# Optimization experiments

Measured on AMD Instinct MI355X. Metric: run time of the kernel, lower is better.

Reference implementation:

```python
import jax, jax.numpy as jnp
import numpy as np

D = 64       # feature_dim
C = 64       # number of classes
NS = 1024    # support samples (16 shots per class)
NQ = 32768   # query samples
REG = 0.3    # reg_param
KAPPA0 = 1.0 / 600.0  # gamma_m from _num_images=600


def _l2norm(x):
    # torch F.normalize(p=2, dim=1) with eps=1e-12
    return x / jnp.maximum(jnp.linalg.norm(x, axis=1, keepdims=True), 1e-12)


def setup_inputs() -> dict:
    key = jax.random.key(0)
    k1, k2 = jax.random.split(key)
    return {
        "X_support": jax.random.normal(k1, (NS, D), dtype=jnp.float32),
        "y_support": jnp.arange(NS, dtype=jnp.int32) % C,  # every class populated
        "X_query": jax.random.normal(k2, (NQ, D), dtype=jnp.float32),
        "m": jnp.zeros((D,), dtype=jnp.float32),            # zeros * gamma_m
        "S": jnp.eye(D, dtype=jnp.float32),                  # eye * gamma_S
        "nu": jnp.float32(float(D)),
        "kappa": jnp.float32(KAPPA0),
    }


def reference(X_support, y_support, X_query, m, S, nu, kappa):
    # ---- fit ----
    Xs = _l2norm(X_support)                                   # [NS, D]
    onehot = jax.nn.one_hot(y_support, C, dtype=Xs.dtype)     # [NS, C]
    Nj = onehot.sum(axis=0)                                   # [C] per-class counts
    means = (onehot.T @ Xs) / Nj[:, None]                     # [C, D] class means
    N0 = Nj[0]                                                # original uses class-0 count
    # head_mu_eq is vector + scalar broadcast, exactly as the torch code
    head = kappa / (kappa + N0) * m + N0 / (kappa + N0)       # [D]
    mu = head[None, :] * means                                # [C, D] elementwise product
    L = S * jnp.tril(jnp.ones((D, D), dtype=Xs.dtype))        # triu(ones).t() mask
    middle = L @ L.T                                          # [D, D]
    Ssum = jnp.einsum('nj,nd,ne->jde', onehot, Xs, Xs)        # sum of outer products per class
    left = 1.0 / (nu + Nj + D + 2)                            # [C]
    mmT = kappa * jnp.outer(m, m)                             # [D, D]
    mu_outer = jnp.einsum('jd,je->jde', mu, mu)               # [C, D, D]
    right = middle[None] + Ssum + mmT[None] - (kappa + Nj)[:, None, None] * mu_outer
    sigma = left[:, None, None] * right                       # [C, D, D]
    A = (1.0 - REG) * jnp.linalg.inv(sigma) + REG * jnp.eye(D, dtype=Xs.dtype)

    # ---- predict: -(x - mu_j)^T A_j (x - mu_j), A_j symmetric ----
    Xq = _l2norm(X_query)                                     # [NQ, D]
    Amu = jnp.einsum('jde,je->jd', A, mu)                     # [C, D]
    cross = Xq @ Amu.T                                        # [NQ, C]
    muAmu = jnp.einsum('jd,jd->j', mu, Amu)                   # [C]
    XA = jnp.einsum('nd,jde->nje', Xq, A)                     # [NQ, C, D]
    quad = jnp.einsum('nje,ne->nj', XA, Xq)                   # [NQ, C]
    return -(quad - 2.0 * cross + muAmu[None, :])             # [NQ, C]
```

## Files before the change

kernel.cpp:

```cpp
#include <hip/hip_runtime.h>
#include <stdint.h>

#define NSUP 1024
#define NQRY 32768
#define DIM  64
#define NCLS 64

typedef float  f32x4  __attribute__((ext_vector_type(4)));
typedef short  s16x8  __attribute__((ext_vector_type(8)));
typedef __bf16 bf16x8 __attribute__((ext_vector_type(8)));

static __device__ __forceinline__ unsigned short f2bf(float f) {
  unsigned u = __float_as_uint(f);
  u += 0x7FFFu + ((u >> 16) & 1u);
  return (unsigned short)(u >> 16);
}
static __device__ __forceinline__ float bf2f(unsigned short s) {
  return __uint_as_float(((unsigned)s) << 16);
}

__global__ __launch_bounds__(256) void prep_queries(const float* __restrict__ Xq,
                                                    unsigned short* __restrict__ Ybf) {
  int tid  = threadIdx.x;
  int lane = tid & 63;
  int wave = tid >> 6;
  int row  = blockIdx.x * 16 + wave * 4 + (lane >> 4);
  int cb   = (lane & 15) * 4;
  float4 v = *(const float4*)(Xq + row * 64 + cb);
  float ss = v.x * v.x + v.y * v.y + v.z * v.z + v.w * v.w;
  ss += __shfl_xor(ss, 1);
  ss += __shfl_xor(ss, 2);
  ss += __shfl_xor(ss, 4);
  ss += __shfl_xor(ss, 8);
  float inv = 1.0f / fmaxf(sqrtf(ss), 1e-12f);
  unsigned short a = f2bf(v.x * inv), b = f2bf(v.y * inv);
  unsigned short c = f2bf(v.z * inv), d = f2bf(v.w * inv);
  uint2 o;
  o.x = (unsigned)a | ((unsigned)b << 16);
  o.y = (unsigned)c | ((unsigned)d << 16);
  *(uint2*)(Ybf + row * 64 + cb) = o;
}

__global__ __launch_bounds__(256) void fit_classes(
    const float* __restrict__ Xs, const int* __restrict__ ys,
    const float* __restrict__ mg, const float* __restrict__ Sg,
    const float* __restrict__ nug, const float* __restrict__ kapg,
    unsigned short* __restrict__ Abf, float* __restrict__ AmuG,
    float* __restrict__ muAmuG) {
  __shared__ int   yls[NSUP];
  __shared__ float Sls[64 * 66];
  __shared__ float xsch[16][64];
  __shared__ float mls[64];
  __shared__ float muls[64];
  __shared__ float Als[64 * 66];
  __shared__ float fcol[64];
  __shared__ float prow[64];
  __shared__ int   lst[NSUP];
  __shared__ int   cnts[2];

  int tid = threadIdx.x;
  int j   = blockIdx.x;

  for (int i = tid; i < NSUP; i += 256) yls[i] = ys[i];
  for (int i = tid; i < 4096; i += 256) Sls[(i >> 6) * 66 + (i & 63)] = Sg[i];
  if (tid < 64) mls[tid] = mg[tid];
  __syncthreads();

  if (tid < 64) {
    int lane = tid;
    int cnt = 0, n0 = 0;
    for (int b = 0; b < NSUP; b += 64) {
      int yv = yls[b + lane];
      unsigned long long mj = __ballot(yv == j);
      unsigned long long m0 = __ballot(yv == 0);
      if (lane == 0) {
        n0 += (int)__popcll(m0);
        while (mj) { int bit = __builtin_ctzll(mj); lst[cnt++] = b + bit; mj &= mj - 1; }
      }
    }
    if (lane == 0) { cnts[0] = cnt; cnts[1] = n0; }
  }
  __syncthreads();
  int cnt = cnts[0], n0 = cnts[1];

  int r_   = tid & 63;
  int cblk = tid >> 6;
  int c0   = cblk * 16;
  float accS[16];
#pragma unroll
  for (int i = 0; i < 16; ++i) accS[i] = 0.f;
  float sumx = 0.f;

  for (int s0 = 0; s0 < cnt; s0 += 16) {
    int nch = min(16, cnt - s0);
    if (tid < 64) {
      for (int s = 0; s < nch; ++s) {
        int n = lst[s0 + s];
        float v = Xs[n * 64 + tid];
        float ss = v * v;
        ss += __shfl_xor(ss, 1);  ss += __shfl_xor(ss, 2);
        ss += __shfl_xor(ss, 4);  ss += __shfl_xor(ss, 8);
        ss += __shfl_xor(ss, 16); ss += __shfl_xor(ss, 32);
        float inv = 1.0f / fmaxf(sqrtf(ss), 1e-12f);
        xsch[s][tid] = v * inv;
      }
    }
    __syncthreads();
    for (int s = 0; s < nch; ++s) {
      float a = xsch[s][r_];
      if (cblk == 0) sumx += a;
#pragma unroll
      for (int i = 0; i < 16; ++i) accS[i] += a * xsch[s][c0 + i];
    }
    __syncthreads();
  }

  float kap = kapg[0];
  float nuv = nug[0];
  if (tid < 64) {
    float Njf = (float)cnt, N0f = (float)n0;
    float mean = sumx / Njf;
    float head = kap / (kap + N0f) * mls[tid] + N0f / (kap + N0f);
    muls[tid] = head * mean;
  }
  __syncthreads();

  {
    float Njf  = (float)cnt;
    float left = 1.0f / (nuv + Njf + (float)DIM + 2.0f);
    float kn   = kap + Njf;
    float mr   = mls[r_], mur = muls[r_];
#pragma unroll 1
    for (int i = 0; i < 16; ++i) {
      int c = c0 + i;
      int kmax = min(r_, c);
      float mid = 0.f;
      for (int k = 0; k <= kmax; ++k) mid += Sls[r_ * 66 + k] * Sls[c * 66 + k];
      float val = mid + accS[i] + kap * mr * mls[c] - kn * mur * muls[c];
      Als[r_ * 66 + c] = left * val;
    }
  }
  __syncthreads();

  int rr  = tid >> 2;
  int cq  = tid & 3;
  int cc0 = cq * 16;
  for (int p = 0; p < 64; ++p) {
    if (cq == (p >> 4)) fcol[rr] = Als[rr * 66 + p];
    if (rr == p) {
#pragma unroll
      for (int i = 0; i < 16; ++i) prow[cc0 + i] = Als[p * 66 + cc0 + i];
    }
    __syncthreads();
    float d  = 1.0f / fcol[p];
    float fr = fcol[rr];
#pragma unroll
    for (int i = 0; i < 16; ++i) {
      int c = cc0 + i;
      float q  = prow[c] * d;
      float ar = Als[rr * 66 + c];
      float res;
      if (rr == p) res = (c == p) ? d : q;
      else         res = (c == p) ? (-fr * d) : fmaf(-fr, q, ar);
      Als[rr * 66 + c] = res;
    }
    __syncthreads();
  }

  {
    unsigned short tmp[16];
#pragma unroll
    for (int i = 0; i < 16; ++i) {
      int c = cc0 + i;
      float a = 0.7f * Als[rr * 66 + c] + ((c == rr) ? 0.3f : 0.0f);
      tmp[i] = f2bf(a);
    }
    uint4 w0, w1;
    w0.x = (unsigned)tmp[0]  | ((unsigned)tmp[1]  << 16);
    w0.y = (unsigned)tmp[2]  | ((unsigned)tmp[3]  << 16);
    w0.z = (unsigned)tmp[4]  | ((unsigned)tmp[5]  << 16);
    w0.w = (unsigned)tmp[6]  | ((unsigned)tmp[7]  << 16);
    w1.x = (unsigned)tmp[8]  | ((unsigned)tmp[9]  << 16);
    w1.y = (unsigned)tmp[10] | ((unsigned)tmp[11] << 16);
    w1.z = (unsigned)tmp[12] | ((unsigned)tmp[13] << 16);
    w1.w = (unsigned)tmp[14] | ((unsigned)tmp[15] << 16);
    *(uint4*)(Abf + j * 4096 + rr * 64 + cc0)     = w0;
    *(uint4*)(Abf + j * 4096 + rr * 64 + cc0 + 8) = w1;
  }

  if (tid < 64) {
    float s = 0.f;
    for (int c = 0; c < 64; ++c) s += Als[tid * 66 + c] * muls[c];
    float amu = 0.7f * s + 0.3f * muls[tid];
    AmuG[j * 64 + tid] = amu;
    float t2 = amu * muls[tid];
    t2 += __shfl_xor(t2, 1);  t2 += __shfl_xor(t2, 2);
    t2 += __shfl_xor(t2, 4);  t2 += __shfl_xor(t2, 8);
    t2 += __shfl_xor(t2, 16); t2 += __shfl_xor(t2, 32);
    if (tid == 0) muAmuG[j] = t2;
  }
}

__global__ __launch_bounds__(512, 2) void predict_kernel(
    const unsigned short* __restrict__ Ybf, const unsigned short* __restrict__ Abf,
    const float* __restrict__ AmuG, const float* __restrict__ muAmuG,
    float* __restrict__ out) {
  __shared__ __align__(16) unsigned short Albuf[2][4096];
  int tid   = threadIdx.x;
  int lane  = tid & 63;
  int wave  = tid >> 6;
  int qt    = blockIdx.x >> 2;
  int cg    = blockIdx.x & 3;
  int cbase = cg * 16;
  int qbase = qt * 512 + wave * 64;
  int c = lane & 15, h = lane >> 4;

  s16x8 bfr[4][2];
  float yc[4][4][4];
#pragma unroll
  for (int nt = 0; nt < 4; ++nt) {
    const unsigned short* yrow = Ybf + (size_t)(qbase + nt * 16 + c) * 64;
#pragma unroll
    for (int ks = 0; ks < 2; ++ks)
      bfr[nt][ks] = *(const s16x8*)(yrow + ks * 32 + h * 8);
#pragma unroll
    for (int et = 0; et < 4; ++et) {
      uint2 u = *(const uint2*)(yrow + et * 16 + h * 4);
      yc[nt][et][0] = bf2f((unsigned short)(u.x & 0xFFFFu));
      yc[nt][et][1] = bf2f((unsigned short)(u.x >> 16));
      yc[nt][et][2] = bf2f((unsigned short)(u.y & 0xFFFFu));
      yc[nt][et][3] = bf2f((unsigned short)(u.y >> 16));
    }
  }

  {
    uint4 v = *(const uint4*)(Abf + (size_t)cbase * 4096 + tid * 8);
    *(uint4*)&Albuf[0][tid * 8] = v;
  }
  __syncthreads();

  float sc[16];
  int cur = 0;
#pragma unroll
  for (int jj = 0; jj < 16; ++jj) {
    int jcls = cbase + jj;
    uint4 stg;
    if (jj < 15) stg = *(const uint4*)(Abf + (size_t)(jcls + 1) * 4096 + tid * 8);

    s16x8 af[4][2];
#pragma unroll
    for (int et = 0; et < 4; ++et)
#pragma unroll
      for (int ks = 0; ks < 2; ++ks)
        af[et][ks] = *(const s16x8*)&Albuf[cur][(et * 16 + c) * 64 + ks * 32 + h * 8];

    float am[4][4];
#pragma unroll
    for (int et = 0; et < 4; ++et) {
      float4 a4 = *(const float4*)(AmuG + jcls * 64 + et * 16 + h * 4);
      am[et][0] = a4.x; am[et][1] = a4.y; am[et][2] = a4.z; am[et][3] = a4.w;
    }
    float mua = muAmuG[jcls];

    float p[4];
#pragma unroll
    for (int nt = 0; nt < 4; ++nt) {
      f32x4 acc[4];
#pragma unroll
      for (int et = 0; et < 4; ++et) acc[et] = (f32x4){0.f, 0.f, 0.f, 0.f};
#pragma unroll
      for (int ks = 0; ks < 2; ++ks)
#pragma unroll
        for (int et = 0; et < 4; ++et)
          acc[et] = __builtin_amdgcn_mfma_f32_16x16x32_bf16(
              __builtin_bit_cast(bf16x8, af[et][ks]),
              __builtin_bit_cast(bf16x8, bfr[nt][ks]), acc[et], 0, 0, 0);
      float s = 0.f;
#pragma unroll
      for (int et = 0; et < 4; ++et)
#pragma unroll
        for (int r = 0; r < 4; ++r)
          s += (acc[et][r] - 2.0f * am[et][r]) * yc[nt][et][r];
      s += __shfl_xor(s, 16);
      s += __shfl_xor(s, 32);
      p[nt] = s;
    }
    float ps = (h == 0) ? p[0] : (h == 1) ? p[1] : (h == 2) ? p[2] : p[3];
    sc[jj] = -ps - mua;

    if (jj < 15) *(uint4*)&Albuf[cur ^ 1][tid * 8] = stg;
    __syncthreads();
    cur ^= 1;
  }

  float* orow = out + (size_t)(qbase + lane) * 64 + cbase;
#pragma unroll
  for (int k = 0; k < 4; ++k) {
    f32x4 v = { sc[4 * k], sc[4 * k + 1], sc[4 * k + 2], sc[4 * k + 3] };
    *(f32x4*)(orow + 4 * k) = v;
  }
}

extern "C" void kernel_launch(void* const* d_in, const int* in_sizes, int n_in,
                              void* d_out, int out_size, void* d_ws, size_t ws_size,
                              hipStream_t stream) {
  const float* Xs   = (const float*)d_in[0];
  const int*   ys   = (const int*)d_in[1];
  const float* Xq   = (const float*)d_in[2];
  const float* mg   = (const float*)d_in[3];
  const float* Sg   = (const float*)d_in[4];
  const float* nug  = (const float*)d_in[5];
  const float* kapg = (const float*)d_in[6];
  float* out = (float*)d_out;

  unsigned short* Ybf = (unsigned short*)d_ws;
  unsigned short* Abf = Ybf + (size_t)NQRY * 64;
  float* AmuG   = (float*)(Abf + (size_t)NCLS * 4096);
  float* muAmuG = AmuG + NCLS * 64;

  prep_queries<<<dim3(NQRY / 16), dim3(256), 0, stream>>>(Xq, Ybf);
  fit_classes<<<dim3(NCLS), dim3(256), 0, stream>>>(Xs, ys, mg, Sg, nug, kapg,
                                                    Abf, AmuG, muAmuG);
  predict_kernel<<<dim3(256), dim3(512), 0, stream>>>(Ybf, Abf, AmuG, muAmuG, out);
}
```

Baseline: 352.7 us.

## Cholesky-factor A per class and compute predict score as squared norm

The fit kernel now Cholesky-factors each class precision matrix A = L L^T and stores L^T in bf16 together with B = L^T mu. The predict kernel then scores each query as -||L^T x - L^T mu||^2: it exploits the triangular structure to issue 6 MFMAs per tile instead of 8, and drops the elementwise y*acc pass and the muAmu term. Class matrices are now prefetched straight into registers rather than double-buffered through LDS with barriers, and the launch uses 256-thread blocks. The trade-off is a serial 64-step Cholesky in the fit kernel and different rounding, since L is quantized to bf16 instead of A.

Result: slower. 408.8 us (+15.9%).

```diff
diff --git a/kernel.cpp b/kernel.cpp
--- a/kernel.cpp
+++ b/kernel.cpp
@@ -14,9 +14,6 @@
   unsigned u = __float_as_uint(f);
   u += 0x7FFFu + ((u >> 16) & 1u);
   return (unsigned short)(u >> 16);
-}
-static __device__ __forceinline__ float bf2f(unsigned short s) {
-  return __uint_as_float(((unsigned)s) << 16);
 }
 
 __global__ __launch_bounds__(256) void prep_queries(const float* __restrict__ Xq,
@@ -45,8 +42,7 @@
     const float* __restrict__ Xs, const int* __restrict__ ys,
     const float* __restrict__ mg, const float* __restrict__ Sg,
     const float* __restrict__ nug, const float* __restrict__ kapg,
-    unsigned short* __restrict__ Abf, float* __restrict__ AmuG,
-    float* __restrict__ muAmuG) {
+    unsigned short* __restrict__ LtG, float* __restrict__ Bg) {
   __shared__ int   yls[NSUP];
   __shared__ float Sls[64 * 66];
   __shared__ float xsch[16][64];
@@ -167,13 +163,41 @@
     __syncthreads();
   }
 
+#pragma unroll
+  for (int i = 0; i < 16; ++i) {
+    int c = cc0 + i;
+    float a = 0.7f * Als[rr * 66 + c] + ((c == rr) ? 0.3f : 0.0f);
+    Als[rr * 66 + c] = a;
+  }
+  __syncthreads();
+
+  for (int k = 0; k < 64; ++k) {
+    if (tid < 64) {
+      float dv = Als[k * 66 + k];
+      float rs = 1.0f / sqrtf(dv);
+      float v  = (tid >= k) ? Als[tid * 66 + k] * rs : 0.f;
+      Als[tid * 66 + k] = v;
+      fcol[tid] = v;
+    }
+    __syncthreads();
+    float lr = fcol[rr];
+    if (rr > k) {
+#pragma unroll
+      for (int i = 0; i < 16; ++i) {
+        int cc = cc0 + i;
+        if (cc > k) Als[rr * 66 + cc] -= lr * fcol[cc];
+      }
+    }
+    __syncthreads();
+  }
+
   {
     unsigned short tmp[16];
 #pragma unroll
     for (int i = 0; i < 16; ++i) {
-      int c = cc0 + i;
-      float a = 0.7f * Als[rr * 66 + c] + ((c == rr) ? 0.3f : 0.0f);
-      tmp[i] = f2bf(a);
+      int d = cc0 + i;
+      float v = (d >= rr) ? Als[d * 66 + rr] : 0.f;
+      tmp[i] = f2bf(v);
     }
     uint4 w0, w1;
     w0.x = (unsigned)tmp[0]  | ((unsigned)tmp[1]  << 16);
@@ -184,113 +208,94 @@
     w1.y = (unsigned)tmp[10] | ((unsigned)tmp[11] << 16);
     w1.z = (unsigned)tmp[12] | ((unsigned)tmp[13] << 16);
     w1.w = (unsigned)tmp[14] | ((unsigned)tmp[15] << 16);
-    *(uint4*)(Abf + j * 4096 + rr * 64 + cc0)     = w0;
-    *(uint4*)(Abf + j * 4096 + rr * 64 + cc0 + 8) = w1;
+    *(uint4*)(LtG + j * 4096 + rr * 64 + cc0)     = w0;
+    *(uint4*)(LtG + j * 4096 + rr * 64 + cc0 + 8) = w1;
   }
 
   if (tid < 64) {
     float s = 0.f;
-    for (int c = 0; c < 64; ++c) s += Als[tid * 66 + c] * muls[c];
-    float amu = 0.7f * s + 0.3f * muls[tid];
-    AmuG[j * 64 + tid] = amu;
-    float t2 = amu * muls[tid];
-    t2 += __shfl_xor(t2, 1);  t2 += __shfl_xor(t2, 2);
-    t2 += __shfl_xor(t2, 4);  t2 += __shfl_xor(t2, 8);
-    t2 += __shfl_xor(t2, 16); t2 += __shfl_xor(t2, 32);
-    if (tid == 0) muAmuG[j] = t2;
-  }
-}
-
-__global__ __launch_bounds__(512, 2) void predict_kernel(
-    const unsigned short* __restrict__ Ybf, const unsigned short* __restrict__ Abf,
-    const float* __restrict__ AmuG, const float* __restrict__ muAmuG,
-    float* __restrict__ out) {
-  __shared__ __align__(16) unsigned short Albuf[2][4096];
+    for (int d = tid; d < 64; ++d) s += Als[d * 66 + tid] * muls[d];
+    Bg[j * 64 + tid] = s;
+  }
+}
+
+__global__ __launch_bounds__(256) void predict_kernel(
+    const unsigned short* __restrict__ Ybf, const unsigned short* __restrict__ Lt,
+    const float* __restrict__ Bg, float* __restrict__ out) {
   int tid   = threadIdx.x;
   int lane  = tid & 63;
   int wave  = tid >> 6;
   int qt    = blockIdx.x >> 2;
   int cg    = blockIdx.x & 3;
   int cbase = cg * 16;
-  int qbase = qt * 512 + wave * 64;
+  int qbase = qt * 256 + wave * 64;
   int c = lane & 15, h = lane >> 4;
 
   s16x8 bfr[4][2];
-  float yc[4][4][4];
 #pragma unroll
   for (int nt = 0; nt < 4; ++nt) {
     const unsigned short* yrow = Ybf + (size_t)(qbase + nt * 16 + c) * 64;
 #pragma unroll
     for (int ks = 0; ks < 2; ++ks)
       bfr[nt][ks] = *(const s16x8*)(yrow + ks * 32 + h * 8);
-#pragma unroll
-    for (int et = 0; et < 4; ++et) {
-      uint2 u = *(const uint2*)(yrow + et * 16 + h * 4);
-      yc[nt][et][0] = bf2f((unsigned short)(u.x & 0xFFFFu));
-      yc[nt][et][1] = bf2f((unsigned short)(u.x >> 16));
-      yc[nt][et][2] = bf2f((unsigned short)(u.y & 0xFFFFu));
-      yc[nt][et][3] = bf2f((unsigned short)(u.y >> 16));
-    }
-  }
-
-  {
-    uint4 v = *(const uint4*)(Abf + (size_t)cbase * 4096 + tid * 8);
-    *(uint4*)&Albuf[0][tid * 8] = v;
-  }
-  __syncthreads();
+  }
+
+  const unsigned short* ab = Lt + (size_t)cbase * 4096 + c * 64 + h * 8;
+  s16x8 af0 = *(const s16x8*)(ab + 0);
+  s16x8 af1 = *(const s16x8*)(ab + 1024);
+  s16x8 af2 = *(const s16x8*)(ab + 32);
+  s16x8 af3 = *(const s16x8*)(ab + 1056);
+  s16x8 af4 = *(const s16x8*)(ab + 2080);
+  s16x8 af5 = *(const s16x8*)(ab + 3104);
 
   float sc[16];
-  int cur = 0;
 #pragma unroll
   for (int jj = 0; jj < 16; ++jj) {
-    int jcls = cbase + jj;
-    uint4 stg;
-    if (jj < 15) stg = *(const uint4*)(Abf + (size_t)(jcls + 1) * 4096 + tid * 8);
-
-    s16x8 af[4][2];
-#pragma unroll
-    for (int et = 0; et < 4; ++et)
-#pragma unroll
-      for (int ks = 0; ks < 2; ++ks)
-        af[et][ks] = *(const s16x8*)&Albuf[cur][(et * 16 + c) * 64 + ks * 32 + h * 8];
-
-    float am[4][4];
-#pragma unroll
-    for (int et = 0; et < 4; ++et) {
-      float4 a4 = *(const float4*)(AmuG + jcls * 64 + et * 16 + h * 4);
-      am[et][0] = a4.x; am[et][1] = a4.y; am[et][2] = a4.z; am[et][3] = a4.w;
-    }
-    float mua = muAmuG[jcls];
-
-    float p[4];
+    s16x8 an0, an1, an2, an3, an4, an5;
+    if (jj < 15) {
+      const unsigned short* an = ab + (size_t)(jj + 1) * 4096;
+      an0 = *(const s16x8*)(an + 0);
+      an1 = *(const s16x8*)(an + 1024);
+      an2 = *(const s16x8*)(an + 32);
+      an3 = *(const s16x8*)(an + 1056);
+      an4 = *(const s16x8*)(an + 2080);
+      an5 = *(const s16x8*)(an + 3104);
+    }
+    const float* bb = Bg + (size_t)(cbase + jj) * 64 + h * 4;
+    float4 b0 = *(const float4*)(bb);
+    float4 b1 = *(const float4*)(bb + 16);
+    float4 b2 = *(const float4*)(bb + 32);
+    float4 b3 = *(const float4*)(bb + 48);
+
+    float ssel = 0.f;
 #pragma unroll
     for (int nt = 0; nt < 4; ++nt) {
-      f32x4 acc[4];
-#pragma unroll
-      for (int et = 0; et < 4; ++et) acc[et] = (f32x4){0.f, 0.f, 0.f, 0.f};
-#pragma unroll
-      for (int ks = 0; ks < 2; ++ks)
-#pragma unroll
-        for (int et = 0; et < 4; ++et)
-          acc[et] = __builtin_amdgcn_mfma_f32_16x16x32_bf16(
-              __builtin_bit_cast(bf16x8, af[et][ks]),
-              __builtin_bit_cast(bf16x8, bfr[nt][ks]), acc[et], 0, 0, 0);
-      float s = 0.f;
-#pragma unroll
-      for (int et = 0; et < 4; ++et)
-#pragma unroll
-        for (int r = 0; r < 4; ++r)
-          s += (acc[et][r] - 2.0f * am[et][r]) * yc[nt][et][r];
+      f32x4 a0 = {-b0.x, -b0.y, -b0.z, -b0.w};
+      f32x4 a1 = {-b1.x, -b1.y, -b1.z, -b1.w};
+      f32x4 a2 = {-b2.x, -b2.y, -b2.z, -b2.w};
+      f32x4 a3 = {-b3.x, -b3.y, -b3.z, -b3.w};
+      a0 = __builtin_amdgcn_mfma_f32_16x16x32_bf16(
+          __builtin_bit_cast(bf16x8, af0), __builtin_bit_cast(bf16x8, bfr[nt][0]), a0, 0, 0, 0);
+      a1 = __builtin_amdgcn_mfma_f32_16x16x32_bf16(
+          __builtin_bit_cast(bf16x8, af1), __builtin_bit_cast(bf16x8, bfr[nt][0]), a1, 0, 0, 0);
+      a0 = __builtin_amdgcn_mfma_f32_16x16x32_bf16(
+          __builtin_bit_cast(bf16x8, af2), __builtin_bit_cast(bf16x8, bfr[nt][1]), a0, 0, 0, 0);
+      a1 = __builtin_amdgcn_mfma_f32_16x16x32_bf16(
+          __builtin_bit_cast(bf16x8, af3), __builtin_bit_cast(bf16x8, bfr[nt][1]), a1, 0, 0, 0);
+      a2 = __builtin_amdgcn_mfma_f32_16x16x32_bf16(
+          __builtin_bit_cast(bf16x8, af4), __builtin_bit_cast(bf16x8, bfr[nt][1]), a2, 0, 0, 0);
+      a3 = __builtin_amdgcn_mfma_f32_16x16x32_bf16(
+          __builtin_bit_cast(bf16x8, af5), __builtin_bit_cast(bf16x8, bfr[nt][1]), a3, 0, 0, 0);
+      float s = a0[0] * a0[0] + a0[1] * a0[1] + a0[2] * a0[2] + a0[3] * a0[3];
+      s += a1[0] * a1[0] + a1[1] * a1[1] + a1[2] * a1[2] + a1[3] * a1[3];
+      s += a2[0] * a2[0] + a2[1] * a2[1] + a2[2] * a2[2] + a2[3] * a2[3];
+      s += a3[0] * a3[0] + a3[1] * a3[1] + a3[2] * a3[2] + a3[3] * a3[3];
       s += __shfl_xor(s, 16);
       s += __shfl_xor(s, 32);
-      p[nt] = s;
-    }
-    float ps = (h == 0) ? p[0] : (h == 1) ? p[1] : (h == 2) ? p[2] : p[3];
-    sc[jj] = -ps - mua;
-
-    if (jj < 15) *(uint4*)&Albuf[cur ^ 1][tid * 8] = stg;
-    __syncthreads();
-    cur ^= 1;
+      if (nt == h) ssel = s;
+    }
+    sc[jj] = -ssel;
+    if (jj < 15) { af0 = an0; af1 = an1; af2 = an2; af3 = an3; af4 = an4; af5 = an5; }
   }
 
   float* orow = out + (size_t)(qbase + lane) * 64 + cbase;
@@ -314,12 +319,11 @@
   float* out = (float*)d_out;
 
   unsigned short* Ybf = (unsigned short*)d_ws;
-  unsigned short* Abf = Ybf + (size_t)NQRY * 64;
-  float* AmuG   = (float*)(Abf + (size_t)NCLS * 4096);
-  float* muAmuG = AmuG + NCLS * 64;
+  unsigned short* LtG = Ybf + (size_t)NQRY * 64;
+  float* Bg = (float*)(LtG + (size_t)NCLS * 4096);
 
   prep_queries<<<dim3(NQRY / 16), dim3(256), 0, stream>>>(Xq, Ybf);
   fit_classes<<<dim3(NCLS), dim3(256), 0, stream>>>(Xs, ys, mg, Sg, nug, kapg,
-                                                    Abf, AmuG, muAmuG);
-  predict_kernel<<<dim3(256), dim3(512), 0, stream>>>(Ybf, Abf, AmuG, muAmuG, out);
-}
+                                                    LtG, Bg);
+  predict_kernel<<<dim3(512), dim3(256), 0, stream>>>(Ybf, LtG, Bg, out);
+}
```
